# Kernel optimization log

Measured on AMD Instinct MI355X. Metric: run time of the kernel, lower is better.

## Reference

```python
import jax, jax.numpy as jnp
import numpy as np

EMBED_DIM = 768
NUM_HEAD = 12
HEAD_DIM = 64
SCALE = 1.0 / np.sqrt(HEAD_DIM)


def setup_inputs() -> dict:
    key = jax.random.key(0)
    k1, k2, k3, k4 = jax.random.split(key, 4)
    B, T = 2, 2048
    x = jax.random.normal(k1, (B, T, EMBED_DIM), dtype=jnp.float32)
    # nn.Linear(embed_dim, 3*embed_dim, bias=True): weight [3E, E], bias [3E]
    w_qkv = jax.random.normal(k2, (3 * EMBED_DIM, EMBED_DIM), dtype=jnp.float32) * (1.0 / np.sqrt(EMBED_DIM))
    b_qkv = jax.random.normal(k3, (3 * EMBED_DIM,), dtype=jnp.float32) * 0.02
    # nn.Linear(embed_dim, embed_dim, bias=False): weight [E, E]
    w_final = jax.random.normal(k4, (EMBED_DIM, EMBED_DIM), dtype=jnp.float32) * (1.0 / np.sqrt(EMBED_DIM))
    return {"x": x, "w_qkv": w_qkv, "b_qkv": b_qkv, "w_final": w_final}


def reference(x, w_qkv, b_qkv, w_final):
    B, T, E = x.shape
    # qkv projection: x @ W^T + b  -> [B, T, 3E]
    qkv = jnp.einsum('bte,fe->btf', x, w_qkv) + b_qkv
    q, k, v = jnp.split(qkv, 3, axis=-1)

    def heads(t):  # [B, T, E] -> [B, H, T, D]
        return t.reshape(B, T, NUM_HEAD, HEAD_DIM).transpose(0, 2, 1, 3)

    q, k, v = heads(q), heads(k), heads(v)
    # scores [B, H, T, T]
    scores = jnp.einsum('bhtd,bhsd->bhts', q, k) * SCALE
    causal = jnp.tril(jnp.ones((T, T), dtype=bool))
    scores = jnp.where(causal, scores, -jnp.inf)
    attn = jax.nn.softmax(scores, axis=-1)  # dropout off (eval mode)
    out = jnp.einsum('bhts,bhsd->bhtd', attn, v)  # [B, H, T, D]
    out = out.transpose(0, 2, 1, 3).reshape(B, T, NUM_HEAD * HEAD_DIM)
    return jnp.einsum('bte,fe->btf', out, w_final)
```

## Files before the change

### kernel.cpp

```cpp
#include <hip/hip_runtime.h>
#include <cstdint>

typedef _Float16 f16x8 __attribute__((ext_vector_type(8)));
typedef _Float16 f16x4 __attribute__((ext_vector_type(4)));
typedef float    f32x4 __attribute__((ext_vector_type(4)));

static constexpr int TB = 2;
static constexpr int TT = 2048;
static constexpr int TE = 768;
static constexpr int TH = 12;
static constexpr int TD = 64;
static constexpr int TM = TB * TT;
static constexpr int TK = TE;
static constexpr int NQKV = 3 * TE;

#define SCALE_LOG2E 0.18033688011112042f

__device__ __forceinline__ void gload16(const void* g, void* lds) {
  __builtin_amdgcn_global_load_lds(
      (__attribute__((address_space(1))) void*)(uintptr_t)g,
      (__attribute__((address_space(3))) void*)(uint32_t)(uintptr_t)lds, 16, 0, 0);
}

__global__ void cvt3(const float* __restrict__ x, const float* __restrict__ wq,
                     const float* __restrict__ wf, _Float16* __restrict__ xh,
                     _Float16* __restrict__ wqh, _Float16* __restrict__ wfh) {
  const int NX = TM * TK / 4, NW = NQKV * TK / 4;
  int i = blockIdx.x * 256 + threadIdx.x;
  const float4* src; _Float16* dst; int j;
  if (i < NX)            { src = (const float4*)x;  dst = xh;  j = i; }
  else if (i < NX + NW)  { src = (const float4*)wq; dst = wqh; j = i - NX; }
  else                   { src = (const float4*)wf; dst = wfh; j = i - NX - NW; }
  float4 v = src[j];
  f16x4 o = {(_Float16)v.x, (_Float16)v.y, (_Float16)v.z, (_Float16)v.w};
  *(f16x4*)&dst[(size_t)j * 4] = o;
}

template <int EPI, int NXT>
__global__ __launch_bounds__(512)
void gemm_nt(const _Float16* __restrict__ A, const _Float16* __restrict__ Bw,
             const float* __restrict__ bias,
             _Float16* __restrict__ qb, _Float16* __restrict__ kb,
             _Float16* __restrict__ vtb, float* __restrict__ outp) {
  __shared__ _Float16 As[2][128 * 64];
  __shared__ _Float16 Bs[2][128 * 64];
  const int tid = threadIdx.x;
  const int w = tid >> 6, lane = tid & 63;
  const int lr = lane & 15, lk = lane >> 4;

  const int id = blockIdx.x;
  const int xcd = id & 7, j = id >> 3;
  const int m0 = (xcd * 4 + j / NXT) * 128;
  const int n0 = (j % NXT) * 128;
  const int wr = w >> 2, wc = w & 3;

  f32x4 acc[4][2] = {};
  const char* Ab = (const char*)(A + (size_t)m0 * TK);
  const char* Bb = (const char*)(Bw + (size_t)n0 * TK);
  const char* Tb = (w < 4) ? Ab : Bb;

  auto stage = [&](int k0, int buf) {
    char* Ls = (char*)((w < 4) ? As[buf] : Bs[buf]);
#pragma unroll
    for (int c = 0; c < 4; ++c) {
      int g = (w & 3) * 4 + c;
      int o = g * 1024 + lane * 16;
      int row = o >> 7, ch = (o >> 4) & 7;
      gload16(Tb + (size_t)row * (TK * 2) + k0 * 2 + ((ch ^ (row & 7)) << 4),
              Ls + g * 1024);
    }
  };

  constexpr int NS = TK / 64;
  stage(0, 0);
  for (int ks = 0; ks < NS; ++ks) {
    const int cur = ks & 1;
    if (ks + 1 < NS) {
      stage((ks + 1) * 64, cur ^ 1);
      asm volatile("s_waitcnt vmcnt(4)" ::: "memory");
    } else {
      asm volatile("s_waitcnt vmcnt(0)" ::: "memory");
    }
    __builtin_amdgcn_s_barrier();

#pragma unroll
    for (int kc = 0; kc < 2; ++kc) {
      f16x8 af[4], bf[2];
#pragma unroll
      for (int mi = 0; mi < 4; ++mi) {
        int row = wr * 64 + mi * 16 + lr;
        af[mi] =
            *(const f16x8*)&As[cur][row * 64 + (((kc * 4 + lk) ^ (row & 7)) << 3)];
      }
#pragma unroll
      for (int ni = 0; ni < 2; ++ni) {
        int row = wc * 32 + ni * 16 + lr;
        bf[ni] =
            *(const f16x8*)&Bs[cur][row * 64 + (((kc * 4 + lk) ^ (row & 7)) << 3)];
      }
#pragma unroll
      for (int mi = 0; mi < 4; ++mi)
#pragma unroll
        for (int ni = 0; ni < 2; ++ni)
          acc[mi][ni] = __builtin_amdgcn_mfma_f32_16x16x32_f16(af[mi], bf[ni],
                                                               acc[mi][ni], 0, 0, 0);
    }
    __builtin_amdgcn_s_barrier();
  }

#pragma unroll
  for (int mi = 0; mi < 4; ++mi) {
#pragma unroll
    for (int ni = 0; ni < 2; ++ni) {
      const int col = n0 + wc * 32 + ni * 16 + lr;
#pragma unroll
      for (int r = 0; r < 4; ++r) {
        const int row = m0 + wr * 64 + mi * 16 + lk * 4 + r;
        float v = acc[mi][ni][r];
        if (EPI == 0) {
          v += bias[col];
          const int which = (col >= 2 * TE) ? 2 : (col >= TE ? 1 : 0);
          const int e = col - which * TE;
          const int h = e >> 6, d = e & 63;
          const int b = row >> 11, t = row & (TT - 1);
          const size_t hb = (size_t)(b * TH + h);
          if (which == 0) {
            qb[(hb * TT + t) * TD + d] = (_Float16)(v * SCALE_LOG2E);
          } else if (which == 1) {
            kb[((((hb * 128 + (t >> 4)) * 8 + (d >> 3)) * 16 + (t & 15)) * 8) +
               (d & 7)] = (_Float16)v;
          } else {
            const int kc = (t >> 5) & 1, hi = (t >> 4) & 1;
            const int lkv = (t >> 2) & 3, m = t & 3;
            vtb[((((((hb * 32 + (t >> 6)) * 4 + (d >> 4)) * 2 + kc) * 4 + lkv) *
                      16 +
                  (d & 15)) *
                 8) +
                (hi * 4 + m)] = (_Float16)v;
          }
        } else {
          outp[(size_t)row * TE + col] = v;
        }
      }
    }
  }
}

__global__ __launch_bounds__(256)
void attn_kernel(const _Float16* __restrict__ qbuf, const _Float16* __restrict__ kbuf,
                 const _Float16* __restrict__ vtbuf, _Float16* __restrict__ ob) {
  const int tid = threadIdx.x, w = tid >> 6, lane = tid & 63;
  const int lr = lane & 15, lk = lane >> 4;

  const int id = blockIdx.x;
  const int bh = id % 24;
  const int qt = 31 - id / 24;
  const int t0 = qt * 64;
  const int nt = qt + 1, ntm1 = qt;

  const _Float16* q = qbuf + (size_t)bh * (TT * TD);
  const char* kbase =
      (const char*)(kbuf + (size_t)bh * (TT * TD)) + lk * 256 + lr * 16;
  const char* vbase =
      (const char*)(vtbuf + (size_t)bh * (TT * TD)) + lk * 256 + lr * 16;

  f16x8 qf[2];
#pragma unroll
  for (int kc = 0; kc < 2; ++kc)
    qf[kc] = *(const f16x8*)&q[(size_t)(t0 + w * 16 + lr) * TD + kc * 32 + lk * 8];

  f32x4 of[4] = {};
  float mrun = -1e30f, lrun = 0.f;

  f16x8 kfA[2][4], kfB[2][4], vf[2][4];

#pragma unroll
  for (int kc = 0; kc < 2; ++kc)
#pragma unroll
    for (int ni = 0; ni < 4; ++ni)
      kfA[kc][ni] = *(const f16x8*)(kbase + ni * 2048 + kc * 1024);
  {
    const char* k1 = kbase + (size_t)(nt > 1 ? 1 : 0) * 8192;
#pragma unroll
    for (int kc = 0; kc < 2; ++kc)
#pragma unroll
      for (int ni = 0; ni < 4; ++ni)
        kfB[kc][ni] = *(const f16x8*)(k1 + ni * 2048 + kc * 1024);
  }

  auto phase = [&](f16x8 (&kf)[2][4], int st) {
    const char* vt = vbase + (size_t)st * 8192;
#pragma unroll
    for (int kc = 0; kc < 2; ++kc)
#pragma unroll
      for (int nd = 0; nd < 4; ++nd)
        vf[kc][nd] = *(const f16x8*)(vt + nd * 2048 + kc * 1024);

    f32x4 sa[4] = {};
    __builtin_amdgcn_s_setprio(1);
#pragma unroll
    for (int kc = 0; kc < 2; ++kc)
#pragma unroll
      for (int ni = 0; ni < 4; ++ni)
        sa[ni] =
            __builtin_amdgcn_mfma_f32_16x16x32_f16(kf[kc][ni], qf[kc], sa[ni], 0, 0, 0);
    __builtin_amdgcn_s_setprio(0);

    {
      const int stp = (st + 2 <= ntm1) ? st + 2 : ntm1;
      const char* kt = kbase + (size_t)stp * 8192;
#pragma unroll
      for (int kc = 0; kc < 2; ++kc)
#pragma unroll
        for (int ni = 0; ni < 4; ++ni)
          kf[kc][ni] = *(const f16x8*)(kt + ni * 2048 + kc * 1024);
    }

    if (st == ntm1) {
      const int s0 = st * 64;
#pragma unroll
      for (int ni = 0; ni < 4; ++ni)
#pragma unroll
        for (int r = 0; r < 4; ++r)
          if (s0 + ni * 16 + lk * 4 + r > t0 + w * 16 + lr) sa[ni][r] = -1e30f;
    }

    float mx;
    {
      float m0_ = fmaxf(fmaxf(sa[0][0], sa[0][1]), fmaxf(sa[0][2], sa[0][3]));
      float m1_ = fmaxf(fmaxf(sa[1][0], sa[1][1]), fmaxf(sa[1][2], sa[1][3]));
      float m2_ = fmaxf(fmaxf(sa[2][0], sa[2][1]), fmaxf(sa[2][2], sa[2][3]));
      float m3_ = fmaxf(fmaxf(sa[3][0], sa[3][1]), fmaxf(sa[3][2], sa[3][3]));
      mx = fmaxf(fmaxf(m0_, m1_), fmaxf(m2_, m3_));
      mx = fmaxf(mx, __shfl_xor(mx, 16));
      mx = fmaxf(mx, __shfl_xor(mx, 32));
    }

    if (__any(mx > mrun + 8.0f)) {
      float mn = fmaxf(mrun, mx);
      float al = __builtin_amdgcn_exp2f(mrun - mn);
      mrun = mn;
      lrun *= al;
      float al4[4];
#pragma unroll
      for (int r = 0; r < 4; ++r) al4[r] = __shfl(al, lk * 4 + r);
#pragma unroll
      for (int nd = 0; nd < 4; ++nd)
#pragma unroll
        for (int r = 0; r < 4; ++r) of[nd][r] *= al4[r];
    }

    f16x8 pa[2];
    float rs;
    {
      float rn[4];
#pragma unroll
      for (int ni = 0; ni < 4; ++ni) {
        float p0 = __builtin_amdgcn_exp2f(sa[ni][0] - mrun);
        float p1 = __builtin_amdgcn_exp2f(sa[ni][1] - mrun);
        float p2 = __builtin_amdgcn_exp2f(sa[ni][2] - mrun);
        float p3 = __builtin_amdgcn_exp2f(sa[ni][3] - mrun);
        rn[ni] = (p0 + p1) + (p2 + p3);
        pa[ni >> 1][(ni & 1) * 4 + 0] = (_Float16)p0;
        pa[ni >> 1][(ni & 1) * 4 + 1] = (_Float16)p1;
        pa[ni >> 1][(ni & 1) * 4 + 2] = (_Float16)p2;
        pa[ni >> 1][(ni & 1) * 4 + 3] = (_Float16)p3;
      }
      rs = (rn[0] + rn[1]) + (rn[2] + rn[3]);
      rs += __shfl_xor(rs, 16);
      rs += __shfl_xor(rs, 32);
    }
    lrun += rs;

    __builtin_amdgcn_s_setprio(1);
#pragma unroll
    for (int kc = 0; kc < 2; ++kc)
#pragma unroll
      for (int nd = 0; nd < 4; ++nd)
        of[nd] =
            __builtin_amdgcn_mfma_f32_16x16x32_f16(pa[kc], vf[kc][nd], of[nd], 0, 0, 0);
    __builtin_amdgcn_s_setprio(0);
  };

  int st = 0;
  while (st + 1 < nt) {
    phase(kfA, st);
    phase(kfB, st + 1);
    st += 2;
  }
  if (st < nt) phase(kfA, st);

  float linv[4];
#pragma unroll
  for (int r = 0; r < 4; ++r) linv[r] = __shfl(lrun, lk * 4 + r);
  const int b = bh / TH, h = bh - b * TH;
#pragma unroll
  for (int nd = 0; nd < 4; ++nd) {
#pragma unroll
    for (int r = 0; r < 4; ++r) {
      int tg = t0 + w * 16 + lk * 4 + r;
      int d = nd * 16 + lr;
      ob[(size_t)(b * TT + tg) * TE + h * TD + d] = (_Float16)(of[nd][r] / linv[r]);
    }
  }
}

extern "C" void kernel_launch(void* const* d_in, const int* in_sizes, int n_in,
                              void* d_out, int out_size, void* d_ws, size_t ws_size,
                              hipStream_t stream) {
  const float* x    = (const float*)d_in[0];
  const float* wqkv = (const float*)d_in[1];
  const float* bqkv = (const float*)d_in[2];
  const float* wfin = (const float*)d_in[3];
  float* out = (float*)d_out;

  _Float16* xh  = (_Float16*)d_ws;
  _Float16* wqh = xh + (size_t)TM * TK;
  _Float16* wfh = wqh + (size_t)NQKV * TK;
  _Float16* qb  = wfh + (size_t)TE * TE;
  _Float16* kb  = qb + (size_t)TM * TE;
  _Float16* vtb = kb + (size_t)TM * TE;
  _Float16* ob  = vtb + (size_t)TM * TE;

  cvt3<<<5376, 256, 0, stream>>>(x, wqkv, wfin, xh, wqh, wfh);
  gemm_nt<0, NQKV / 128><<<(NQKV / 128) * (TM / 128), 512, 0, stream>>>(
      xh, wqh, bqkv, qb, kb, vtb, nullptr);
  attn_kernel<<<dim3(TT / 64 * TB * TH), 256, 0, stream>>>(qb, kb, vtb, ob);
  gemm_nt<1, TE / 128><<<(TE / 128) * (TM / 128), 512, 0, stream>>>(
      ob, wfh, nullptr, nullptr, nullptr, nullptr, out);
}
```

Measured before the change: 86.71 us.

## Prelayout GEMM weights into MFMA fragment order and double attention rows per wave

The conversion kernel now writes both weight matrices in a tiled fragment-major layout, so the GEMM loads each wave's B operand straight from global memory into registers. This drops the B shared-memory tile and its double buffer, leaving only A staged through LDS. The attention kernel moves from 4 waves with 16 query rows each to 2 waves with 32 query rows each, so every K fragment load feeds twice as many QK MFMAs. In exchange, B is read from global or L2 by every wave without LDS sharing, and attention uses more registers per wave with half the waves per block.

```diff
diff --git a/kernel.cpp b/kernel.cpp
--- a/kernel.cpp
+++ b/kernel.cpp
@@ -27,13 +27,22 @@
                      _Float16* __restrict__ wqh, _Float16* __restrict__ wfh) {
   const int NX = TM * TK / 4, NW = NQKV * TK / 4;
   int i = blockIdx.x * 256 + threadIdx.x;
-  const float4* src; _Float16* dst; int j;
-  if (i < NX)            { src = (const float4*)x;  dst = xh;  j = i; }
-  else if (i < NX + NW)  { src = (const float4*)wq; dst = wqh; j = i - NX; }
-  else                   { src = (const float4*)wf; dst = wfh; j = i - NX - NW; }
-  float4 v = src[j];
-  f16x4 o = {(_Float16)v.x, (_Float16)v.y, (_Float16)v.z, (_Float16)v.w};
-  *(f16x4*)&dst[(size_t)j * 4] = o;
+  if (i < NX) {
+    float4 v = ((const float4*)x)[i];
+    f16x4 o = {(_Float16)v.x, (_Float16)v.y, (_Float16)v.z, (_Float16)v.w};
+    *(f16x4*)&xh[(size_t)i * 4] = o;
+  } else {
+    const float4* src; _Float16* dst; int j;
+    if (i < NX + NW) { src = (const float4*)wq; dst = wqh; j = i - NX; }
+    else             { src = (const float4*)wf; dst = wfh; j = i - NX - NW; }
+    float4 v = src[j];
+    f16x4 o = {(_Float16)v.x, (_Float16)v.y, (_Float16)v.z, (_Float16)v.w};
+    const int flat = j * 4;
+    const int n = flat / TK, k = flat % TK;
+    const size_t idx = ((size_t)(n >> 4) * 24 + (k >> 5)) * 512 +
+                       ((k >> 3) & 3) * 128 + (n & 15) * 8 + (k & 7);
+    *(f16x4*)&dst[idx] = o;
+  }
 }
 
 template <int EPI, int NXT>
@@ -43,7 +52,6 @@
              _Float16* __restrict__ qb, _Float16* __restrict__ kb,
              _Float16* __restrict__ vtb, float* __restrict__ outp) {
   __shared__ _Float16 As[2][128 * 64];
-  __shared__ _Float16 Bs[2][128 * 64];
   const int tid = threadIdx.x;
   const int w = tid >> 6, lane = tid & 63;
   const int lr = lane & 15, lk = lane >> 4;
@@ -56,56 +64,63 @@
 
   f32x4 acc[4][2] = {};
   const char* Ab = (const char*)(A + (size_t)m0 * TK);
-  const char* Bb = (const char*)(Bw + (size_t)n0 * TK);
-  const char* Tb = (w < 4) ? Ab : Bb;
-
-  auto stage = [&](int k0, int buf) {
-    char* Ls = (char*)((w < 4) ? As[buf] : Bs[buf]);
-#pragma unroll
-    for (int c = 0; c < 4; ++c) {
-      int g = (w & 3) * 4 + c;
+  const char* WB = (const char*)Bw;
+  const int nb = (n0 >> 4) + wc * 2;
+  constexpr int NS = TK / 64;
+
+  auto loadB = [&](int ks, f16x8 (&bf)[2][2]) {
+#pragma unroll
+    for (int ni = 0; ni < 2; ++ni)
+#pragma unroll
+      for (int kc = 0; kc < 2; ++kc)
+        bf[ni][kc] = *(const f16x8*)(WB +
+                                     ((size_t)(nb + ni) * 24 + ks * 2 + kc) * 1024 +
+                                     lane * 16);
+  };
+  auto stageA = [&](int ks, int buf) {
+#pragma unroll
+    for (int c = 0; c < 2; ++c) {
+      int g = w * 2 + c;
       int o = g * 1024 + lane * 16;
       int row = o >> 7, ch = (o >> 4) & 7;
-      gload16(Tb + (size_t)row * (TK * 2) + k0 * 2 + ((ch ^ (row & 7)) << 4),
-              Ls + g * 1024);
-    }
-  };
-
-  constexpr int NS = TK / 64;
-  stage(0, 0);
-  for (int ks = 0; ks < NS; ++ks) {
-    const int cur = ks & 1;
+      gload16(Ab + (size_t)row * (TK * 2) + ks * 128 + ((ch ^ (row & 7)) << 4),
+              (char*)As[buf] + g * 1024);
+    }
+  };
+  auto step = [&](f16x8 (&bc)[2][2], f16x8 (&bn)[2][2], int buf, int ks) {
     if (ks + 1 < NS) {
-      stage((ks + 1) * 64, cur ^ 1);
-      asm volatile("s_waitcnt vmcnt(4)" ::: "memory");
+      loadB(ks + 1, bn);
+      stageA(ks + 1, buf ^ 1);
+      asm volatile("s_waitcnt vmcnt(6)" ::: "memory");
     } else {
       asm volatile("s_waitcnt vmcnt(0)" ::: "memory");
     }
     __builtin_amdgcn_s_barrier();
-
 #pragma unroll
     for (int kc = 0; kc < 2; ++kc) {
-      f16x8 af[4], bf[2];
+      f16x8 af[4];
 #pragma unroll
       for (int mi = 0; mi < 4; ++mi) {
         int row = wr * 64 + mi * 16 + lr;
         af[mi] =
-            *(const f16x8*)&As[cur][row * 64 + (((kc * 4 + lk) ^ (row & 7)) << 3)];
-      }
-#pragma unroll
-      for (int ni = 0; ni < 2; ++ni) {
-        int row = wc * 32 + ni * 16 + lr;
-        bf[ni] =
-            *(const f16x8*)&Bs[cur][row * 64 + (((kc * 4 + lk) ^ (row & 7)) << 3)];
+            *(const f16x8*)&As[buf][row * 64 + (((kc * 4 + lk) ^ (row & 7)) << 3)];
       }
 #pragma unroll
       for (int mi = 0; mi < 4; ++mi)
 #pragma unroll
         for (int ni = 0; ni < 2; ++ni)
-          acc[mi][ni] = __builtin_amdgcn_mfma_f32_16x16x32_f16(af[mi], bf[ni],
+          acc[mi][ni] = __builtin_amdgcn_mfma_f32_16x16x32_f16(af[mi], bc[ni][kc],
                                                                acc[mi][ni], 0, 0, 0);
     }
     __builtin_amdgcn_s_barrier();
+  };
+
+  f16x8 bA[2][2], bB[2][2];
+  loadB(0, bA);
+  stageA(0, 0);
+  for (int kss = 0; kss < NS; kss += 2) {
+    step(bA, bB, 0, kss);
+    step(bB, bA, 1, kss + 1);
   }
 
 #pragma unroll
@@ -146,7 +161,7 @@
   }
 }
 
-__global__ __launch_bounds__(256)
+__global__ __launch_bounds__(128)
 void attn_kernel(const _Float16* __restrict__ qbuf, const _Float16* __restrict__ kbuf,
                  const _Float16* __restrict__ vtbuf, _Float16* __restrict__ ob) {
   const int tid = threadIdx.x, w = tid >> 6, lane = tid & 63;
@@ -157,6 +172,7 @@
   const int qt = 31 - id / 24;
   const int t0 = qt * 64;
   const int nt = qt + 1, ntm1 = qt;
+  const int q0 = t0 + w * 32;
 
   const _Float16* q = qbuf + (size_t)bh * (TT * TD);
   const char* kbase =
@@ -164,13 +180,16 @@
   const char* vbase =
       (const char*)(vtbuf + (size_t)bh * (TT * TD)) + lk * 256 + lr * 16;
 
-  f16x8 qf[2];
-#pragma unroll
-  for (int kc = 0; kc < 2; ++kc)
-    qf[kc] = *(const f16x8*)&q[(size_t)(t0 + w * 16 + lr) * TD + kc * 32 + lk * 8];
-
-  f32x4 of[4] = {};
-  float mrun = -1e30f, lrun = 0.f;
+  f16x8 qf0[2], qf1[2];
+#pragma unroll
+  for (int kc = 0; kc < 2; ++kc) {
+    qf0[kc] = *(const f16x8*)&q[(size_t)(q0 + lr) * TD + kc * 32 + lk * 8];
+    qf1[kc] = *(const f16x8*)&q[(size_t)(q0 + 16 + lr) * TD + kc * 32 + lk * 8];
+  }
+
+  f32x4 of0[4] = {}, of1[4] = {};
+  float mr0 = -1e30f, ls0 = 0.f;
+  float mr1 = -1e30f, ls1 = 0.f;
 
   f16x8 kfA[2][4], kfB[2][4], vf[2][4];
 
@@ -188,78 +207,48 @@
         kfB[kc][ni] = *(const f16x8*)(k1 + ni * 2048 + kc * 1024);
   }
 
-  auto phase = [&](f16x8 (&kf)[2][4], int st) {
-    const char* vt = vbase + (size_t)st * 8192;
-#pragma unroll
-    for (int kc = 0; kc < 2; ++kc)
-#pragma unroll
-      for (int nd = 0; nd < 4; ++nd)
-        vf[kc][nd] = *(const f16x8*)(vt + nd * 2048 + kc * 1024);
-
-    f32x4 sa[4] = {};
-    __builtin_amdgcn_s_setprio(1);
-#pragma unroll
-    for (int kc = 0; kc < 2; ++kc)
+  auto sm_pv = [&](f32x4 (&sa)[4], float& mr, float& ls, f32x4 (&of_)[4],
+                   int qb_, int s0, bool dia) {
+    if (dia) {
 #pragma unroll
       for (int ni = 0; ni < 4; ++ni)
-        sa[ni] =
-            __builtin_amdgcn_mfma_f32_16x16x32_f16(kf[kc][ni], qf[kc], sa[ni], 0, 0, 0);
-    __builtin_amdgcn_s_setprio(0);
-
-    {
-      const int stp = (st + 2 <= ntm1) ? st + 2 : ntm1;
-      const char* kt = kbase + (size_t)stp * 8192;
-#pragma unroll
-      for (int kc = 0; kc < 2; ++kc)
-#pragma unroll
-        for (int ni = 0; ni < 4; ++ni)
-          kf[kc][ni] = *(const f16x8*)(kt + ni * 2048 + kc * 1024);
-    }
-
-    if (st == ntm1) {
-      const int s0 = st * 64;
-#pragma unroll
-      for (int ni = 0; ni < 4; ++ni)
 #pragma unroll
         for (int r = 0; r < 4; ++r)
-          if (s0 + ni * 16 + lk * 4 + r > t0 + w * 16 + lr) sa[ni][r] = -1e30f;
-    }
-
+          if (s0 + ni * 16 + lk * 4 + r > qb_ + lr) sa[ni][r] = -1e30f;
+    }
     float mx;
     {
-      float m0_ = fmaxf(fmaxf(sa[0][0], sa[0][1]), fmaxf(sa[0][2], sa[0][3]));
-      float m1_ = fmaxf(fmaxf(sa[1][0], sa[1][1]), fmaxf(sa[1][2], sa[1][3]));
-      float m2_ = fmaxf(fmaxf(sa[2][0], sa[2][1]), fmaxf(sa[2][2], sa[2][3]));
-      float m3_ = fmaxf(fmaxf(sa[3][0], sa[3][1]), fmaxf(sa[3][2], sa[3][3]));
-      mx = fmaxf(fmaxf(m0_, m1_), fmaxf(m2_, m3_));
+      float a0 = fmaxf(fmaxf(sa[0][0], sa[0][1]), fmaxf(sa[0][2], sa[0][3]));
+      float a1 = fmaxf(fmaxf(sa[1][0], sa[1][1]), fmaxf(sa[1][2], sa[1][3]));
+      float a2 = fmaxf(fmaxf(sa[2][0], sa[2][1]), fmaxf(sa[2][2], sa[2][3]));
+      float a3 = fmaxf(fmaxf(sa[3][0], sa[3][1]), fmaxf(sa[3][2], sa[3][3]));
+      mx = fmaxf(fmaxf(a0, a1), fmaxf(a2, a3));
       mx = fmaxf(mx, __shfl_xor(mx, 16));
       mx = fmaxf(mx, __shfl_xor(mx, 32));
     }
-
-    if (__any(mx > mrun + 8.0f)) {
-      float mn = fmaxf(mrun, mx);
-      float al = __builtin_amdgcn_exp2f(mrun - mn);
-      mrun = mn;
-      lrun *= al;
+    if (__any(mx > mr + 8.0f)) {
+      float mn = fmaxf(mr, mx);
+      float al = __builtin_amdgcn_exp2f(mr - mn);
+      mr = mn;
+      ls *= al;
       float al4[4];
 #pragma unroll
       for (int r = 0; r < 4; ++r) al4[r] = __shfl(al, lk * 4 + r);
 #pragma unroll
       for (int nd = 0; nd < 4; ++nd)
 #pragma unroll
-        for (int r = 0; r < 4; ++r) of[nd][r] *= al4[r];
-    }
-
+        for (int r = 0; r < 4; ++r) of_[nd][r] *= al4[r];
+    }
     f16x8 pa[2];
     float rs;
     {
       float rn[4];
 #pragma unroll
       for (int ni = 0; ni < 4; ++ni) {
-        float p0 = __builtin_amdgcn_exp2f(sa[ni][0] - mrun);
-        float p1 = __builtin_amdgcn_exp2f(sa[ni][1] - mrun);
-        float p2 = __builtin_amdgcn_exp2f(sa[ni][2] - mrun);
-        float p3 = __builtin_amdgcn_exp2f(sa[ni][3] - mrun);
+        float p0 = __builtin_amdgcn_exp2f(sa[ni][0] - mr);
+        float p1 = __builtin_amdgcn_exp2f(sa[ni][1] - mr);
+        float p2 = __builtin_amdgcn_exp2f(sa[ni][2] - mr);
+        float p3 = __builtin_amdgcn_exp2f(sa[ni][3] - mr);
         rn[ni] = (p0 + p1) + (p2 + p3);
         pa[ni >> 1][(ni & 1) * 4 + 0] = (_Float16)p0;
         pa[ni >> 1][(ni & 1) * 4 + 1] = (_Float16)p1;
@@ -270,16 +259,54 @@
       rs += __shfl_xor(rs, 16);
       rs += __shfl_xor(rs, 32);
     }
-    lrun += rs;
-
+    ls += rs;
     __builtin_amdgcn_s_setprio(1);
 #pragma unroll
     for (int kc = 0; kc < 2; ++kc)
 #pragma unroll
       for (int nd = 0; nd < 4; ++nd)
-        of[nd] =
-            __builtin_amdgcn_mfma_f32_16x16x32_f16(pa[kc], vf[kc][nd], of[nd], 0, 0, 0);
+        of_[nd] =
+            __builtin_amdgcn_mfma_f32_16x16x32_f16(pa[kc], vf[kc][nd], of_[nd], 0, 0, 0);
     __builtin_amdgcn_s_setprio(0);
+  };
+
+  auto phase = [&](f16x8 (&kf)[2][4], int st) {
+    const char* vt = vbase + (size_t)st * 8192;
+#pragma unroll
+    for (int kc = 0; kc < 2; ++kc)
+#pragma unroll
+      for (int nd = 0; nd < 4; ++nd)
+        vf[kc][nd] = *(const f16x8*)(vt + nd * 2048 + kc * 1024);
+
+    f32x4 sa0[4] = {}, sa1[4] = {};
+    __builtin_amdgcn_s_setprio(1);
+#pragma unroll
+    for (int kc = 0; kc < 2; ++kc)
+#pragma unroll
+      for (int ni = 0; ni < 4; ++ni)
+        sa0[ni] =
+            __builtin_amdgcn_mfma_f32_16x16x32_f16(kf[kc][ni], qf0[kc], sa0[ni], 0, 0, 0);
+#pragma unroll
+    for (int kc = 0; kc < 2; ++kc)
+#pragma unroll
+      for (int ni = 0; ni < 4; ++ni)
+        sa1[ni] =
+            __builtin_amdgcn_mfma_f32_16x16x32_f16(kf[kc][ni], qf1[kc], sa1[ni], 0, 0, 0);
+    __builtin_amdgcn_s_setprio(0);
+
+    {
+      const int stp = (st + 2 <= ntm1) ? st + 2 : ntm1;
+      const char* kt = kbase + (size_t)stp * 8192;
+#pragma unroll
+      for (int kc = 0; kc < 2; ++kc)
+#pragma unroll
+        for (int ni = 0; ni < 4; ++ni)
+          kf[kc][ni] = *(const f16x8*)(kt + ni * 2048 + kc * 1024);
+    }
+
+    const int s0 = st * 64;
+    sm_pv(sa0, mr0, ls0, of0, q0, s0, s0 + 63 > q0);
+    sm_pv(sa1, mr1, ls1, of1, q0 + 16, s0, s0 + 63 > q0 + 16);
   };
 
   int st = 0;
@@ -290,18 +317,32 @@
   }
   if (st < nt) phase(kfA, st);
 
-  float linv[4];
-#pragma unroll
-  for (int r = 0; r < 4; ++r) linv[r] = __shfl(lrun, lk * 4 + r);
   const int b = bh / TH, h = bh - b * TH;
-#pragma unroll
-  for (int nd = 0; nd < 4; ++nd) {
-#pragma unroll
-    for (int r = 0; r < 4; ++r) {
-      int tg = t0 + w * 16 + lk * 4 + r;
-      int d = nd * 16 + lr;
-      ob[(size_t)(b * TT + tg) * TE + h * TD + d] = (_Float16)(of[nd][r] / linv[r]);
-    }
+  {
+    float linv[4];
+#pragma unroll
+    for (int r = 0; r < 4; ++r) linv[r] = __shfl(ls0, lk * 4 + r);
+#pragma unroll
+    for (int nd = 0; nd < 4; ++nd)
+#pragma unroll
+      for (int r = 0; r < 4; ++r) {
+        int tg = q0 + lk * 4 + r;
+        int d = nd * 16 + lr;
+        ob[(size_t)(b * TT + tg) * TE + h * TD + d] = (_Float16)(of0[nd][r] / linv[r]);
+      }
+  }
+  {
+    float linv[4];
+#pragma unroll
+    for (int r = 0; r < 4; ++r) linv[r] = __shfl(ls1, lk * 4 + r);
+#pragma unroll
+    for (int nd = 0; nd < 4; ++nd)
+#pragma unroll
+      for (int r = 0; r < 4; ++r) {
+        int tg = q0 + 16 + lk * 4 + r;
+        int d = nd * 16 + lr;
+        ob[(size_t)(b * TT + tg) * TE + h * TD + d] = (_Float16)(of1[nd][r] / linv[r]);
+      }
   }
 }
 
@@ -325,7 +366,7 @@
   cvt3<<<5376, 256, 0, stream>>>(x, wqkv, wfin, xh, wqh, wfh);
   gemm_nt<0, NQKV / 128><<<(NQKV / 128) * (TM / 128), 512, 0, stream>>>(
       xh, wqh, bqkv, qb, kb, vtb, nullptr);
-  attn_kernel<<<dim3(TT / 64 * TB * TH), 256, 0, stream>>>(qb, kb, vtb, ob);
+  attn_kernel<<<dim3(TT / 64 * TB * TH), 128, 0, stream>>>(qb, kb, vtb, ob);
   gemm_nt<1, TE / 128><<<(TE / 128) * (TM / 128), 512, 0, stream>>>(
       ob, wfh, nullptr, nullptr, nullptr, nullptr, out);
 }
```

Measured after the change: 93.81 us. 8.2% more time.
